# Performance work log

Hardware: AMD Instinct MI355X
Metric: run time of the kernel (lower is better)

The kernel has to match this reference:

```python
import jax
import jax.numpy as jnp
import numpy as np
from jax import lax

# Model dims (see init_kwargs)
B, C, D, M, L = 16, 64, 128, 16, 3
PROJ, OUT = 64, 1  # projection_size defaults to channels; output_size=1


def _spectral_conv(v, w1, w2, bias):
    """FNO 2D spectral convolution. v: [B,C,D,D]; w1,w2: [C,C,M,M,2] (re/im); bias: [C]."""
    vft = jnp.fft.rfft2(v, norm="backward")            # [B,C,D,D//2+1] complex
    w1c = w1[..., 0] + 1j * w1[..., 1]                   # [C,C,M,M]
    w2c = w2[..., 0] + 1j * w2[..., 1]
    top = jnp.einsum("bixy,ioxy->boxy", vft[:, :, :M, :M], w1c)
    bot = jnp.einsum("bixy,ioxy->boxy", vft[:, :, -M:, :M], w2c)
    out_ft = jnp.zeros_like(vft)
    out_ft = out_ft.at[:, :, :M, :M].set(top).at[:, :, -M:, :M].set(bot)
    out = jnp.fft.irfft2(out_ft, s=(D, D), norm="backward")
    return out + bias[None, :, None, None]               # in_bias


def _rk4(f, z0, ts):
    """Fixed-grid RK4 (torchdiffeq method='rk4'): one step per interval; return final state."""
    def step(z, tp):
        h = tp[1] - tp[0]
        k1 = f(z)
        k2 = f(z + 0.5 * h * k1)
        k3 = f(z + 0.5 * h * k2)
        k4 = f(z + h * k3)
        return z + (h / 6.0) * (k1 + 2.0 * k2 + 2.0 * k3 + k4), None
    pairs = jnp.stack([ts[:-1], ts[1:]], axis=1)         # [T-1, 2]
    zf, _ = lax.scan(step, z0, pairs)
    return zf


def setup_inputs() -> dict:
    key = jax.random.key(0)
    ks = jax.random.split(key, 12)
    scale = 1.0 / C                                       # FNO-style spectral weight scale
    z = jax.random.normal(ks[0], (B, 1, D, D), jnp.float32)
    lift_w = jax.random.normal(ks[1], (C, 1), jnp.float32)
    lift_b = jax.random.normal(ks[2], (C,), jnp.float32) * 0.1
    spec_w1 = jax.random.normal(ks[3], (L, C, C, M, M, 2), jnp.float32) * scale
    spec_w2 = jax.random.normal(ks[4], (L, C, C, M, M, 2), jnp.float32) * scale
    fl_bias = jax.random.normal(ks[5], (L, C), jnp.float32) * 0.1
    p1_w = jax.random.normal(ks[6], (PROJ, C), jnp.float32) / np.sqrt(C)
    p1_b = jax.random.normal(ks[7], (PROJ,), jnp.float32) * 0.1
    p2_w = jax.random.normal(ks[8], (OUT, PROJ), jnp.float32) / np.sqrt(PROJ)
    p2_b = jax.random.normal(ks[9], (OUT,), jnp.float32) * 0.1
    samp_ts = jnp.linspace(0.0, 1.0, 5, dtype=jnp.float32)
    return dict(z=z, lift_w=lift_w, lift_b=lift_b, spec_w1=spec_w1, spec_w2=spec_w2,
                fl_bias=fl_bias, p1_w=p1_w, p1_b=p1_b, p2_w=p2_w, p2_b=p2_b,
                samp_ts=samp_ts)


def reference(z, lift_w, lift_b, spec_w1, spec_w2, fl_bias, p1_w, p1_b, p2_w, p2_b, samp_ts):
    # Lifting: pointwise channel lift 1 -> C
    v = jnp.einsum("bixy,oi->boxy", z, lift_w) + lift_b[None, :, None, None]
    out = v
    # n_layers Fourier layers, each integrated with RK4 over samp_ts; take final time
    for l in range(L):
        f = lambda u, l=l: _spectral_conv(u, spec_w1[l], spec_w2[l], fl_bias[l])
        out = _rk4(f, out, samp_ts)
    # Projection: pointwise C -> PROJ -> OUT
    h = jnp.einsum("bcxy,pc->bpxy", out, p1_w) + p1_b[None, :, None, None]
    out = jnp.einsum("bpxy,op->boxy", h, p2_w) + p2_b[None, :, None, None]
    return out
```

## Files before the change

kernel.cpp:

```cpp
#include <hip/hip_runtime.h>

namespace {

constexpr int kNXI = 33;
constexpr int kNY = 16;
constexpr int kNMODE = kNY * kNXI;
constexpr int kModeBlocks = 265;
constexpr int kFwd1Blocks = 2048;

constexpr int WS_ALPHA = 0;
constexpr int WS_GAMMA = 1;
constexpr int WS_S = 4;
constexpr int WS_ZY = WS_S + kNMODE * 2;
constexpr int WS_T = WS_ZY;

constexpr float kTheta = 0.04908738521234052f;

__device__ __forceinline__ float rl(float v, int i) {
  return __uint_as_float(__builtin_amdgcn_readlane(__float_as_uint(v), i));
}

__device__ __forceinline__ float wave_sum(float v) {
  v += __shfl_xor(v, 1);  v += __shfl_xor(v, 2);  v += __shfl_xor(v, 4);
  v += __shfl_xor(v, 8);  v += __shfl_xor(v, 16); v += __shfl_xor(v, 32);
  return v;
}

__global__ __launch_bounds__(128) void fnde_phase1(
    const float* __restrict__ w1, const float* __restrict__ w2,
    const float* __restrict__ flb, const float* __restrict__ lw,
    const float* __restrict__ lb, const float* __restrict__ ts,
    const float* __restrict__ p1w, const float* __restrict__ p1b,
    const float* __restrict__ p2w, const float* __restrict__ p2b,
    const float* __restrict__ z, float* __restrict__ ws) {
  const int b = blockIdx.x;

  if (b >= kModeBlocks) {
    const int bid = b - kModeBlocks;
    const int bb = bid >> 7, xs = bid & 127;
    const int t = threadIdx.x;
    __shared__ float zrow[128], tc[128], tsn[128], rre[128], rim[128];
    sincosf((float)t * kTheta, &tsn[t], &tc[t]);
    zrow[t] = z[bb * 16384 + xs * 128 + t];
    __syncthreads();
    int y = t & 15, part = t >> 4;
    float sre = 0.f, sim = 0.f;
    for (int j = 0; j < 16; ++j) {
      int ys = (part << 4) + j;
      int k = (y * ys) & 127;
      float zv = zrow[ys];
      sre += zv * tc[k];
      sim -= zv * tsn[k];
    }
    rre[t] = sre; rim[t] = sim;
    __syncthreads();
    if (t < 16) {
      float ar = 0.f, ai = 0.f;
      for (int pp = 0; pp < 8; ++pp) { ar += rre[(pp << 4) + t]; ai += rim[(pp << 4) + t]; }
      int idx = ((bb * 128 + xs) * 16 + t) * 2;
      ws[WS_ZY + idx] = ar; ws[WS_ZY + idx + 1] = ai;
    }
    return;
  }

  const int t = threadIdx.x;
  const int o = t & 63, w = t >> 6;

  const float t0 = ts[0], t1 = ts[1], t2 = ts[2], t3 = ts[3], t4 = ts[4];
  const float h0 = t1 - t0, h1 = t2 - t1, h2 = t3 - t2, h3 = t4 - t3;

  if (b == kModeBlocks - 1) {
    if (w == 1) return;
    float q = 0.f;
    for (int p = 0; p < 64; ++p) q = fmaf(p2w[p], p1w[p * 64 + o], q);
    float e = lb[o];
    const float* lanep = w1 + o * 512;
    for (int l = 0; l < 3; ++l) {
      float Wc[64];
#pragma unroll
      for (int i = 0; i < 64; ++i) Wc[i] = lanep[(size_t)(l * 64 + i) * 32768];
      const float bia = flb[l * 64 + o];
      for (int step = 0; step < 4; ++step) {
        const float h = (step == 0) ? h0 : (step == 1) ? h1 : (step == 2) ? h2 : h3;
        float acc = 0.f, u = e;
        for (int st = 0; st < 4; ++st) {
          float k0 = 0.f, k1 = 0.f;
#pragma unroll
          for (int i = 0; i < 64; i += 2) {
            k0 = fmaf(Wc[i],     rl(u, i),     k0);
            k1 = fmaf(Wc[i + 1], rl(u, i + 1), k1);
          }
          const float k = k0 + k1 + bia;
          const float wsm = (st == 1 || st == 2) ? 2.f : 1.f;
          acc = fmaf(wsm, k, acc);
          if (st < 3) {
            const float cm = (st < 2) ? 0.5f * h : h;
            u = fmaf(cm, k, e);
          } else {
            e = fmaf(h * (1.f / 6.f), acc, e);
          }
        }
      }
    }
    const float g = wave_sum(fmaf(p2w[o], p1b[o], q * e));
    if (o == 0) ws[WS_GAMMA] = g + p2b[0];
    return;
  }

  const int xcd = b & 7, kk0 = (b >> 3) * 2 + w;
  int xi, y;
  if (kk0 < 64) { xi = xcd * 4 + (kk0 >> 4); y = kk0 & 15; }
  else          { xi = 32;                   y = xcd * 2 + (kk0 - 64); }
  const int m = y * kNXI + xi;

  const bool inactive = (y == 0) ? (xi > 16) : (xi == 16);
  if (inactive) {
    if (o == 0) { ws[WS_S + 2 * m] = 0.f; ws[WS_S + 2 * m + 1] = 0.f; }
    return;
  }

  float q = 0.f;
  for (int p = 0; p < 64; ++p) q = fmaf(p2w[p], p1w[p * 64 + o], q);

  float zr = lw[o], zi = 0.f;
  float2 Wc[64];

  for (int l = 0; l < 3; ++l) {
    if (y >= 1) {
      const float* lanep = ((xi <= 15) ? (w1 + (xi * 16 + y) * 2)
                                       : (w2 + ((xi - 17) * 16 + y) * 2)) + o * 512;
#pragma unroll
      for (int i = 0; i < 64; ++i)
        Wc[i] = *reinterpret_cast<const float2*>(lanep + (size_t)(l * 64 + i) * 32768);
    } else {
      const bool hasA = (xi <= 15);
      const float* lanepA = w1 + xi * 32 + o * 512;
      const float* lanepB = (xi >= 1) ? (w2 + (16 - xi) * 32 + o * 512)
                                      : (w1 + o * 512);
#pragma unroll
      for (int i = 0; i < 64; ++i) {
        const float2 a = hasA ? *reinterpret_cast<const float2*>(lanepA + (size_t)(l * 64 + i) * 32768)
                              : make_float2(0.f, 0.f);
        const float2 bb = *reinterpret_cast<const float2*>(lanepB + (size_t)(l * 64 + i) * 32768);
        Wc[i] = make_float2(0.5f * (a.x + bb.x), 0.5f * (a.y - bb.y));
      }
    }

    for (int step = 0; step < 4; ++step) {
      const float h = (step == 0) ? h0 : (step == 1) ? h1 : (step == 2) ? h2 : h3;
      float accr = 0.f, acci = 0.f;
      float ur = zr, ui = zi;
      for (int st = 0; st < 4; ++st) {
        float ar0 = 0.f, ai0 = 0.f, ar1 = 0.f, ai1 = 0.f;
#pragma unroll
        for (int i = 0; i < 64; i += 2) {
          const float x0r = rl(ur, i),     x0i = rl(ui, i);
          const float x1r = rl(ur, i + 1), x1i = rl(ui, i + 1);
          ar0 = fmaf(Wc[i].x,     x0r, ar0);  ar0 = fmaf(-Wc[i].y,     x0i, ar0);
          ai0 = fmaf(Wc[i].x,     x0i, ai0);  ai0 = fmaf(Wc[i].y,     x0r, ai0);
          ar1 = fmaf(Wc[i + 1].x, x1r, ar1);  ar1 = fmaf(-Wc[i + 1].y, x1i, ar1);
          ai1 = fmaf(Wc[i + 1].x, x1i, ai1);  ai1 = fmaf(Wc[i + 1].y,  x1r, ai1);
        }
        const float kr = ar0 + ar1, ki = ai0 + ai1;
        const float wsm = (st == 1 || st == 2) ? 2.f : 1.f;
        accr = fmaf(wsm, kr, accr); acci = fmaf(wsm, ki, acci);
        if (st < 3) {
          const float cm = (st < 2) ? 0.5f * h : h;
          ur = fmaf(cm, kr, zr); ui = fmaf(cm, ki, zi);
        } else {
          zr = fmaf(h * (1.f / 6.f), accr, zr);
          zi = fmaf(h * (1.f / 6.f), acci, zi);
        }
      }
    }
  }

  const float sr = wave_sum(q * (zr - lw[o]));
  const float si = wave_sum(q * zi);
  if (o == 0) { ws[WS_S + 2 * m] = sr; ws[WS_S + 2 * m + 1] = si; }
  if (y == 0 && xi == 0) {
    const float a = wave_sum(q * lw[o]);
    if (o == 0) ws[WS_ALPHA] = a;
  }
}

__global__ void fnde_mid(float* __restrict__ ws) {
  const int b = blockIdx.x >> 4, y = blockIdx.x & 15;
  const int t = threadIdx.x;
  __shared__ float cr[128], ci[128], tc[128], tsn[128], Sre[kNXI], Sim[kNXI];
  sincosf((float)t * kTheta, &tsn[t], &tc[t]);
  int idx = ((b * 128 + t) * 16 + y) * 2;
  cr[t] = ws[WS_ZY + idx]; ci[t] = ws[WS_ZY + idx + 1];
  __syncthreads();
  if (t < kNXI) {
    int x = (t <= 16) ? t : t + 95;
    float ar = 0.f, ai = 0.f;
    for (int xs = 0; xs < 128; ++xs) {
      int k = (x * xs) & 127;
      float c = tc[k], s = tsn[k];
      ar += cr[xs] * c + ci[xs] * s;
      ai += ci[xs] * c - cr[xs] * s;
    }
    int mm = y * kNXI + t;
    float sr = ws[WS_S + 2 * mm], si = ws[WS_S + 2 * mm + 1];
    Sre[t] = sr * ar - si * ai;
    Sim[t] = sr * ai + si * ar;
  }
  __syncthreads();
  const int xs = t;
  float ar, ai;
  if (y > 0) {
    ar = 0.f; ai = 0.f;
    for (int xj = 0; xj < kNXI; ++xj) {
      int x = (xj <= 16) ? xj : xj + 95;
      int k = (x * xs) & 127;
      float c = tc[k], s = tsn[k];
      ar += Sre[xj] * c - Sim[xj] * s;
      ai += Sre[xj] * s + Sim[xj] * c;
    }
  } else {
    ar = Sre[0]; ai = 0.f;
    for (int xj = 1; xj <= 16; ++xj) {
      int k = (xj * xs) & 127;
      ar += 2.f * (Sre[xj] * tc[k] - Sim[xj] * tsn[k]);
    }
  }
  ws[WS_T + idx] = ar; ws[WS_T + idx + 1] = ai;
}

__global__ void fnde_final(const float* __restrict__ z, const float* __restrict__ ws,
                           float* __restrict__ out) {
  const int bid = blockIdx.x;
  const int b = bid >> 7, xs = bid & 127;
  const int t = threadIdx.x;
  __shared__ float Tre[16], Tim[16], tc[128], tsn[128];
  sincosf((float)t * kTheta, &tsn[t], &tc[t]);
  if (t < 16) {
    int idx = ((b * 128 + xs) * 16 + t) * 2;
    Tre[t] = ws[WS_T + idx]; Tim[t] = ws[WS_T + idx + 1];
  }
  __syncthreads();
  float acc = Tre[0];
  for (int y = 1; y < 16; ++y) {
    int k = (y * t) & 127;
    acc += 2.f * (Tre[y] * tc[k] - Tim[y] * tsn[k]);
  }
  float val = ws[WS_ALPHA] * z[b * 16384 + xs * 128 + t] + ws[WS_GAMMA]
            + acc * (1.f / 16384.f);
  out[b * 16384 + xs * 128 + t] = val;
}

}

extern "C" void kernel_launch(void* const* d_in, const int* in_sizes, int n_in,
                              void* d_out, int out_size, void* d_ws, size_t ws_size,
                              hipStream_t stream) {
  (void)in_sizes; (void)n_in; (void)out_size; (void)ws_size;
  const float* z   = (const float*)d_in[0];
  const float* lw  = (const float*)d_in[1];
  const float* lb  = (const float*)d_in[2];
  const float* w1  = (const float*)d_in[3];
  const float* w2  = (const float*)d_in[4];
  const float* flb = (const float*)d_in[5];
  const float* p1w = (const float*)d_in[6];
  const float* p1b = (const float*)d_in[7];
  const float* p2w = (const float*)d_in[8];
  const float* p2b = (const float*)d_in[9];
  const float* ts  = (const float*)d_in[10];
  float* ws = (float*)d_ws;
  float* out = (float*)d_out;

  fnde_phase1<<<dim3(kModeBlocks + kFwd1Blocks), dim3(128), 0, stream>>>(
      w1, w2, flb, lw, lb, ts, p1w, p1b, p2w, p2b, z, ws);
  fnde_mid<<<dim3(256), dim3(128), 0, stream>>>(ws);
  fnde_final<<<dim3(2048), dim3(128), 0, stream>>>(z, ws, out);
}
```

Measured before the change: 94.57 us.

## Split per-mode channel matvec across four waves with LDS reduction

Each mode block now uses four waves, each holding 16 of the 64 input-channel weights instead of one wave holding all 64. Partial complex dot products are exchanged through shared memory with a barrier every RK4 stage, replacing readlane broadcasts. This cuts per-thread register use and serial FMA chain length so more waves can run in parallel. The forward-row blocks are also doubled up to two rows per block. The cost is a __syncthreads per stage (48 per block) and twice as many mode blocks.

```diff
diff --git a/kernel.cpp b/kernel.cpp
--- a/kernel.cpp
+++ b/kernel.cpp
@@ -5,8 +5,8 @@
 constexpr int kNXI = 33;
 constexpr int kNY = 16;
 constexpr int kNMODE = kNY * kNXI;
-constexpr int kModeBlocks = 265;
-constexpr int kFwd1Blocks = 2048;
+constexpr int kModeBlocks = 529;
+constexpr int kFwd1Blocks = 1024;
 
 constexpr int WS_ALPHA = 0;
 constexpr int WS_GAMMA = 1;
@@ -16,17 +16,13 @@
 
 constexpr float kTheta = 0.04908738521234052f;
 
-__device__ __forceinline__ float rl(float v, int i) {
-  return __uint_as_float(__builtin_amdgcn_readlane(__float_as_uint(v), i));
-}
-
 __device__ __forceinline__ float wave_sum(float v) {
   v += __shfl_xor(v, 1);  v += __shfl_xor(v, 2);  v += __shfl_xor(v, 4);
   v += __shfl_xor(v, 8);  v += __shfl_xor(v, 16); v += __shfl_xor(v, 32);
   return v;
 }
 
-__global__ __launch_bounds__(128) void fnde_phase1(
+__global__ __launch_bounds__(256) void fnde_phase1(
     const float* __restrict__ w1, const float* __restrict__ w2,
     const float* __restrict__ flb, const float* __restrict__ lw,
     const float* __restrict__ lb, const float* __restrict__ ts,
@@ -34,153 +30,151 @@
     const float* __restrict__ p2w, const float* __restrict__ p2b,
     const float* __restrict__ z, float* __restrict__ ws) {
   const int b = blockIdx.x;
+  const int t = threadIdx.x;
 
   if (b >= kModeBlocks) {
+    __shared__ float zrow2[2][128], tcf[128], tsnf[128], rre2[2][128], rim2[2][128];
     const int bid = b - kModeBlocks;
-    const int bb = bid >> 7, xs = bid & 127;
-    const int t = threadIdx.x;
-    __shared__ float zrow[128], tc[128], tsn[128], rre[128], rim[128];
-    sincosf((float)t * kTheta, &tsn[t], &tc[t]);
-    zrow[t] = z[bb * 16384 + xs * 128 + t];
+    const int r = t >> 7, tt = t & 127;
+    const int row = bid * 2 + r;
+    const int bb = row >> 7, xs = row & 127;
+    if (r == 0) sincosf((float)tt * kTheta, &tsnf[tt], &tcf[tt]);
+    zrow2[r][tt] = z[bb * 16384 + xs * 128 + tt];
     __syncthreads();
-    int y = t & 15, part = t >> 4;
+    int y = tt & 15, part = tt >> 4;
     float sre = 0.f, sim = 0.f;
     for (int j = 0; j < 16; ++j) {
       int ys = (part << 4) + j;
       int k = (y * ys) & 127;
-      float zv = zrow[ys];
-      sre += zv * tc[k];
-      sim -= zv * tsn[k];
-    }
-    rre[t] = sre; rim[t] = sim;
+      float zv = zrow2[r][ys];
+      sre += zv * tcf[k];
+      sim -= zv * tsnf[k];
+    }
+    rre2[r][tt] = sre; rim2[r][tt] = sim;
     __syncthreads();
-    if (t < 16) {
+    if (tt < 16) {
       float ar = 0.f, ai = 0.f;
-      for (int pp = 0; pp < 8; ++pp) { ar += rre[(pp << 4) + t]; ai += rim[(pp << 4) + t]; }
-      int idx = ((bb * 128 + xs) * 16 + t) * 2;
+      for (int pp = 0; pp < 8; ++pp) { ar += rre2[r][(pp << 4) + tt]; ai += rim2[r][(pp << 4) + tt]; }
+      int idx = (row * 16 + tt) * 2;
       ws[WS_ZY + idx] = ar; ws[WS_ZY + idx + 1] = ai;
     }
     return;
   }
 
-  const int t = threadIdx.x;
-  const int o = t & 63, w = t >> 6;
+  const int w = t >> 6, o = t & 63;
+  const bool isBias = (b == kModeBlocks - 1);
+
+  int xi = 0, y = 0, m = 0;
+  if (!isBias) {
+    const int xcd = b & 7, k = b >> 3;
+    if (k < 64) { xi = xcd * 4 + (k >> 4); y = k & 15; }
+    else        { xi = 32;                 y = xcd * 2 + (k - 64); }
+    m = y * kNXI + xi;
+    const bool inactive = (y == 0) ? (xi > 16) : (xi == 16);
+    if (inactive) {
+      if (t == 0) { ws[WS_S + 2 * m] = 0.f; ws[WS_S + 2 * m + 1] = 0.f; }
+      return;
+    }
+  }
+
+  __shared__ float2 ubuf[4][64];
+  __shared__ float2 pbuf[2][4][64];
 
   const float t0 = ts[0], t1 = ts[1], t2 = ts[2], t3 = ts[3], t4 = ts[4];
   const float h0 = t1 - t0, h1 = t2 - t1, h2 = t3 - t2, h3 = t4 - t3;
 
-  if (b == kModeBlocks - 1) {
-    if (w == 1) return;
-    float q = 0.f;
+  float q = 0.f;
+  if (w == 0) {
     for (int p = 0; p < 64; ++p) q = fmaf(p2w[p], p1w[p * 64 + o], q);
-    float e = lb[o];
-    const float* lanep = w1 + o * 512;
-    for (int l = 0; l < 3; ++l) {
-      float Wc[64];
-#pragma unroll
-      for (int i = 0; i < 64; ++i) Wc[i] = lanep[(size_t)(l * 64 + i) * 32768];
-      const float bia = flb[l * 64 + o];
-      for (int step = 0; step < 4; ++step) {
-        const float h = (step == 0) ? h0 : (step == 1) ? h1 : (step == 2) ? h2 : h3;
-        float acc = 0.f, u = e;
-        for (int st = 0; st < 4; ++st) {
-          float k0 = 0.f, k1 = 0.f;
-#pragma unroll
-          for (int i = 0; i < 64; i += 2) {
-            k0 = fmaf(Wc[i],     rl(u, i),     k0);
-            k1 = fmaf(Wc[i + 1], rl(u, i + 1), k1);
-          }
-          const float k = k0 + k1 + bia;
-          const float wsm = (st == 1 || st == 2) ? 2.f : 1.f;
-          acc = fmaf(wsm, k, acc);
-          if (st < 3) {
-            const float cm = (st < 2) ? 0.5f * h : h;
-            u = fmaf(cm, k, e);
-          } else {
-            e = fmaf(h * (1.f / 6.f), acc, e);
-          }
-        }
-      }
-    }
-    const float g = wave_sum(fmaf(p2w[o], p1b[o], q * e));
-    if (o == 0) ws[WS_GAMMA] = g + p2b[0];
-    return;
-  }
-
-  const int xcd = b & 7, kk0 = (b >> 3) * 2 + w;
-  int xi, y;
-  if (kk0 < 64) { xi = xcd * 4 + (kk0 >> 4); y = kk0 & 15; }
-  else          { xi = 32;                   y = xcd * 2 + (kk0 - 64); }
-  const int m = y * kNXI + xi;
-
-  const bool inactive = (y == 0) ? (xi > 16) : (xi == 16);
-  if (inactive) {
-    if (o == 0) { ws[WS_S + 2 * m] = 0.f; ws[WS_S + 2 * m + 1] = 0.f; }
-    return;
-  }
-
-  float q = 0.f;
-  for (int p = 0; p < 64; ++p) q = fmaf(p2w[p], p1w[p * 64 + o], q);
-
-  float zr = lw[o], zi = 0.f;
-  float2 Wc[64];
+  }
+
+  float zr = isBias ? lb[o] : lw[o], zi = 0.f;
+  ubuf[w][o] = make_float2(zr, zi);
+
+  int pb = 0;
+  float2 Wc[16];
 
   for (int l = 0; l < 3; ++l) {
-    if (y >= 1) {
+    if (isBias) {
+      const float* lanep = w1 + o * 512;
+#pragma unroll
+      for (int j = 0; j < 16; ++j)
+        Wc[j] = make_float2(lanep[(size_t)(l * 64 + 16 * w + j) * 32768], 0.f);
+    } else if (y >= 1) {
       const float* lanep = ((xi <= 15) ? (w1 + (xi * 16 + y) * 2)
                                        : (w2 + ((xi - 17) * 16 + y) * 2)) + o * 512;
 #pragma unroll
-      for (int i = 0; i < 64; ++i)
-        Wc[i] = *reinterpret_cast<const float2*>(lanep + (size_t)(l * 64 + i) * 32768);
+      for (int j = 0; j < 16; ++j)
+        Wc[j] = *reinterpret_cast<const float2*>(lanep + (size_t)(l * 64 + 16 * w + j) * 32768);
     } else {
       const bool hasA = (xi <= 15);
       const float* lanepA = w1 + xi * 32 + o * 512;
       const float* lanepB = (xi >= 1) ? (w2 + (16 - xi) * 32 + o * 512)
                                       : (w1 + o * 512);
 #pragma unroll
-      for (int i = 0; i < 64; ++i) {
-        const float2 a = hasA ? *reinterpret_cast<const float2*>(lanepA + (size_t)(l * 64 + i) * 32768)
+      for (int j = 0; j < 16; ++j) {
+        const size_t ioff = (size_t)(l * 64 + 16 * w + j) * 32768;
+        const float2 a = hasA ? *reinterpret_cast<const float2*>(lanepA + ioff)
                               : make_float2(0.f, 0.f);
-        const float2 bb = *reinterpret_cast<const float2*>(lanepB + (size_t)(l * 64 + i) * 32768);
-        Wc[i] = make_float2(0.5f * (a.x + bb.x), 0.5f * (a.y - bb.y));
+        const float2 bb2 = *reinterpret_cast<const float2*>(lanepB + ioff);
+        Wc[j] = make_float2(0.5f * (a.x + bb2.x), 0.5f * (a.y - bb2.y));
       }
     }
+    const float bia = isBias ? flb[l * 64 + o] : 0.f;
 
     for (int step = 0; step < 4; ++step) {
       const float h = (step == 0) ? h0 : (step == 1) ? h1 : (step == 2) ? h2 : h3;
       float accr = 0.f, acci = 0.f;
-      float ur = zr, ui = zi;
       for (int st = 0; st < 4; ++st) {
-        float ar0 = 0.f, ai0 = 0.f, ar1 = 0.f, ai1 = 0.f;
-#pragma unroll
-        for (int i = 0; i < 64; i += 2) {
-          const float x0r = rl(ur, i),     x0i = rl(ui, i);
-          const float x1r = rl(ur, i + 1), x1i = rl(ui, i + 1);
-          ar0 = fmaf(Wc[i].x,     x0r, ar0);  ar0 = fmaf(-Wc[i].y,     x0i, ar0);
-          ai0 = fmaf(Wc[i].x,     x0i, ai0);  ai0 = fmaf(Wc[i].y,     x0r, ai0);
-          ar1 = fmaf(Wc[i + 1].x, x1r, ar1);  ar1 = fmaf(-Wc[i + 1].y, x1i, ar1);
-          ai1 = fmaf(Wc[i + 1].x, x1i, ai1);  ai1 = fmaf(Wc[i + 1].y,  x1r, ai1);
+        float2 x[16];
+#pragma unroll
+        for (int jj = 0; jj < 8; ++jj)
+          *reinterpret_cast<float4*>(&x[2 * jj]) =
+              *reinterpret_cast<const float4*>(&ubuf[w][16 * w + 2 * jj]);
+        float pr0 = 0.f, pi0 = 0.f, pr1 = 0.f, pi1 = 0.f;
+#pragma unroll
+        for (int j = 0; j < 16; j += 2) {
+          pr0 = fmaf(Wc[j].x,     x[j].x,     pr0);  pr0 = fmaf(-Wc[j].y,     x[j].y,     pr0);
+          pi0 = fmaf(Wc[j].x,     x[j].y,     pi0);  pi0 = fmaf(Wc[j].y,      x[j].x,     pi0);
+          pr1 = fmaf(Wc[j + 1].x, x[j + 1].x, pr1);  pr1 = fmaf(-Wc[j + 1].y, x[j + 1].y, pr1);
+          pi1 = fmaf(Wc[j + 1].x, x[j + 1].y, pi1);  pi1 = fmaf(Wc[j + 1].y,  x[j + 1].x, pi1);
         }
-        const float kr = ar0 + ar1, ki = ai0 + ai1;
+        pbuf[pb][w][o] = make_float2(pr0 + pr1, pi0 + pi1);
+        __syncthreads();
+        const float2 q0 = pbuf[pb][0][o], q1 = pbuf[pb][1][o];
+        const float2 q2 = pbuf[pb][2][o], q3 = pbuf[pb][3][o];
+        const float kr = q0.x + q1.x + q2.x + q3.x + bia;
+        const float ki = q0.y + q1.y + q2.y + q3.y;
         const float wsm = (st == 1 || st == 2) ? 2.f : 1.f;
         accr = fmaf(wsm, kr, accr); acci = fmaf(wsm, ki, acci);
+        float ur, ui;
         if (st < 3) {
           const float cm = (st < 2) ? 0.5f * h : h;
           ur = fmaf(cm, kr, zr); ui = fmaf(cm, ki, zi);
         } else {
           zr = fmaf(h * (1.f / 6.f), accr, zr);
           zi = fmaf(h * (1.f / 6.f), acci, zi);
+          ur = zr; ui = zi;
         }
+        ubuf[w][o] = make_float2(ur, ui);
+        pb ^= 1;
       }
     }
   }
 
-  const float sr = wave_sum(q * (zr - lw[o]));
-  const float si = wave_sum(q * zi);
-  if (o == 0) { ws[WS_S + 2 * m] = sr; ws[WS_S + 2 * m + 1] = si; }
-  if (y == 0 && xi == 0) {
-    const float a = wave_sum(q * lw[o]);
-    if (o == 0) ws[WS_ALPHA] = a;
+  if (w == 0) {
+    if (isBias) {
+      const float g = wave_sum(fmaf(p2w[o], p1b[o], q * zr));
+      if (o == 0) ws[WS_GAMMA] = g + p2b[0];
+    } else {
+      const float sr = wave_sum(q * (zr - lw[o]));
+      const float si = wave_sum(q * zi);
+      if (o == 0) { ws[WS_S + 2 * m] = sr; ws[WS_S + 2 * m + 1] = si; }
+      if (m == 0) {
+        const float a = wave_sum(q * lw[o]);
+        if (o == 0) ws[WS_ALPHA] = a;
+      }
+    }
   }
 }
 
@@ -270,7 +264,7 @@
   float* ws = (float*)d_ws;
   float* out = (float*)d_out;
 
-  fnde_phase1<<<dim3(kModeBlocks + kFwd1Blocks), dim3(128), 0, stream>>>(
+  fnde_phase1<<<dim3(kModeBlocks + kFwd1Blocks), dim3(256), 0, stream>>>(
       w1, w2, flb, lw, lb, ts, p1w, p1b, p2w, p2b, z, ws);
   fnde_mid<<<dim3(256), dim3(128), 0, stream>>>(ws);
   fnde_final<<<dim3(2048), dim3(128), 0, stream>>>(z, ws, out);
```

Result: no change. 94.48 us (-0.1%).

## Use one-wave blocks and LDS broadcast instead of readlane in mode RK4

Applied to the files above, without the earlier changes.

Each phase-1 block is now a single 64-lane wave, and the number of mode blocks is doubled so each block handles one Fourier mode. Inside the per-mode RK4 matvec, the per-lane readlane broadcasts are replaced by each lane writing its state into shared memory and all lanes reading it back as float4 vectors. The forward row-DFT blocks also shrink to 64 threads, with the partial-sum reduction done by cross-lane shuffles instead of a shared-memory pass. The aim is to avoid the serialized scalar readlane path and to spread work over more blocks. The cost is more LDS traffic, and correctness relies on in-wave ordering of LDS accesses because there is no barrier.

```diff
diff --git a/kernel.cpp b/kernel.cpp
--- a/kernel.cpp
+++ b/kernel.cpp
@@ -5,7 +5,7 @@
 constexpr int kNXI = 33;
 constexpr int kNY = 16;
 constexpr int kNMODE = kNY * kNXI;
-constexpr int kModeBlocks = 265;
+constexpr int kModeBlocks = 529;
 constexpr int kFwd1Blocks = 2048;
 
 constexpr int WS_ALPHA = 0;
@@ -16,17 +16,13 @@
 
 constexpr float kTheta = 0.04908738521234052f;
 
-__device__ __forceinline__ float rl(float v, int i) {
-  return __uint_as_float(__builtin_amdgcn_readlane(__float_as_uint(v), i));
-}
-
 __device__ __forceinline__ float wave_sum(float v) {
   v += __shfl_xor(v, 1);  v += __shfl_xor(v, 2);  v += __shfl_xor(v, 4);
   v += __shfl_xor(v, 8);  v += __shfl_xor(v, 16); v += __shfl_xor(v, 32);
   return v;
 }
 
-__global__ __launch_bounds__(128) void fnde_phase1(
+__global__ __launch_bounds__(64, 1) void fnde_phase1(
     const float* __restrict__ w1, const float* __restrict__ w2,
     const float* __restrict__ flb, const float* __restrict__ lw,
     const float* __restrict__ lb, const float* __restrict__ ts,
@@ -34,71 +30,84 @@
     const float* __restrict__ p2w, const float* __restrict__ p2b,
     const float* __restrict__ z, float* __restrict__ ws) {
   const int b = blockIdx.x;
+  const int o = threadIdx.x;
 
   if (b >= kModeBlocks) {
-    const int bid = b - kModeBlocks;
-    const int bb = bid >> 7, xs = bid & 127;
-    const int t = threadIdx.x;
-    __shared__ float zrow[128], tc[128], tsn[128], rre[128], rim[128];
-    sincosf((float)t * kTheta, &tsn[t], &tc[t]);
-    zrow[t] = z[bb * 16384 + xs * 128 + t];
-    __syncthreads();
-    int y = t & 15, part = t >> 4;
+    __shared__ float zrow[128], tcf[128], tsnf[128];
+    const int row = b - kModeBlocks;
+    const int bb = row >> 7, xs = row & 127;
+    sincosf((float)o * kTheta, &tsnf[o], &tcf[o]);
+    sincosf((float)(o + 64) * kTheta, &tsnf[o + 64], &tcf[o + 64]);
+    const float* zp = z + bb * 16384 + xs * 128;
+    zrow[o] = zp[o]; zrow[o + 64] = zp[o + 64];
+    const int y = o & 15, part = o >> 4;
     float sre = 0.f, sim = 0.f;
-    for (int j = 0; j < 16; ++j) {
-      int ys = (part << 4) + j;
-      int k = (y * ys) & 127;
-      float zv = zrow[ys];
-      sre += zv * tc[k];
-      sim -= zv * tsn[k];
-    }
-    rre[t] = sre; rim[t] = sim;
-    __syncthreads();
-    if (t < 16) {
-      float ar = 0.f, ai = 0.f;
-      for (int pp = 0; pp < 8; ++pp) { ar += rre[(pp << 4) + t]; ai += rim[(pp << 4) + t]; }
-      int idx = ((bb * 128 + xs) * 16 + t) * 2;
-      ws[WS_ZY + idx] = ar; ws[WS_ZY + idx + 1] = ai;
+    for (int j = 0; j < 32; ++j) {
+      const int ys = (part << 5) + j;
+      const int k = (y * ys) & 127;
+      const float zv = zrow[ys];
+      sre = fmaf(zv, tcf[k], sre);
+      sim = fmaf(-zv, tsnf[k], sim);
+    }
+    sre += __shfl_xor(sre, 16); sre += __shfl_xor(sre, 32);
+    sim += __shfl_xor(sim, 16); sim += __shfl_xor(sim, 32);
+    if (o < 16) {
+      const int idx = (row * 16 + o) * 2;
+      ws[WS_ZY + idx] = sre; ws[WS_ZY + idx + 1] = sim;
     }
     return;
   }
 
-  const int t = threadIdx.x;
-  const int o = t & 63, w = t >> 6;
+  const bool isBias = (b == kModeBlocks - 1);
+
+  int xi = 0, y = 0, m = 0;
+  if (!isBias) {
+    const int xcd = b & 7, k = b >> 3;
+    if (k < 64) { xi = xcd * 4 + (k >> 4); y = k & 15; }
+    else        { xi = 32;                 y = xcd * 2 + (k - 64); }
+    m = y * kNXI + xi;
+    const bool inactive = (y == 0) ? (xi > 16) : (xi == 16);
+    if (inactive) {
+      if (o == 0) { ws[WS_S + 2 * m] = 0.f; ws[WS_S + 2 * m + 1] = 0.f; }
+      return;
+    }
+  }
+
+  __shared__ __align__(16) float2 xb[64];
 
   const float t0 = ts[0], t1 = ts[1], t2 = ts[2], t3 = ts[3], t4 = ts[4];
   const float h0 = t1 - t0, h1 = t2 - t1, h2 = t3 - t2, h3 = t4 - t3;
 
-  if (b == kModeBlocks - 1) {
-    if (w == 1) return;
-    float q = 0.f;
-    for (int p = 0; p < 64; ++p) q = fmaf(p2w[p], p1w[p * 64 + o], q);
+  float q = 0.f;
+  for (int p = 0; p < 64; ++p) q = fmaf(p2w[p], p1w[p * 64 + o], q);
+
+  if (isBias) {
     float e = lb[o];
+    xb[o] = make_float2(e, 0.f);
     const float* lanep = w1 + o * 512;
     for (int l = 0; l < 3; ++l) {
-      float Wc[64];
-#pragma unroll
-      for (int i = 0; i < 64; ++i) Wc[i] = lanep[(size_t)(l * 64 + i) * 32768];
+      float Wr[64];
+#pragma unroll
+      for (int i = 0; i < 64; ++i) Wr[i] = lanep[(size_t)(l * 64 + i) * 32768];
       const float bia = flb[l * 64 + o];
       for (int step = 0; step < 4; ++step) {
         const float h = (step == 0) ? h0 : (step == 1) ? h1 : (step == 2) ? h2 : h3;
-        float acc = 0.f, u = e;
+        float acc = 0.f;
         for (int st = 0; st < 4; ++st) {
           float k0 = 0.f, k1 = 0.f;
 #pragma unroll
-          for (int i = 0; i < 64; i += 2) {
-            k0 = fmaf(Wc[i],     rl(u, i),     k0);
-            k1 = fmaf(Wc[i + 1], rl(u, i + 1), k1);
+          for (int ii = 0; ii < 64; ii += 2) {
+            const float4 xx = *reinterpret_cast<const float4*>(&xb[ii]);
+            k0 = fmaf(Wr[ii],     xx.x, k0);
+            k1 = fmaf(Wr[ii + 1], xx.z, k1);
           }
-          const float k = k0 + k1 + bia;
+          const float kk = k0 + k1 + bia;
           const float wsm = (st == 1 || st == 2) ? 2.f : 1.f;
-          acc = fmaf(wsm, k, acc);
-          if (st < 3) {
-            const float cm = (st < 2) ? 0.5f * h : h;
-            u = fmaf(cm, k, e);
-          } else {
-            e = fmaf(h * (1.f / 6.f), acc, e);
-          }
+          acc = fmaf(wsm, kk, acc);
+          float u;
+          if (st < 3) { const float cm = (st < 2) ? 0.5f * h : h; u = fmaf(cm, kk, e); }
+          else        { e = fmaf(h * (1.f / 6.f), acc, e); u = e; }
+          xb[o] = make_float2(u, 0.f);
         }
       }
     }
@@ -107,22 +116,9 @@
     return;
   }
 
-  const int xcd = b & 7, kk0 = (b >> 3) * 2 + w;
-  int xi, y;
-  if (kk0 < 64) { xi = xcd * 4 + (kk0 >> 4); y = kk0 & 15; }
-  else          { xi = 32;                   y = xcd * 2 + (kk0 - 64); }
-  const int m = y * kNXI + xi;
-
-  const bool inactive = (y == 0) ? (xi > 16) : (xi == 16);
-  if (inactive) {
-    if (o == 0) { ws[WS_S + 2 * m] = 0.f; ws[WS_S + 2 * m + 1] = 0.f; }
-    return;
-  }
-
-  float q = 0.f;
-  for (int p = 0; p < 64; ++p) q = fmaf(p2w[p], p1w[p * 64 + o], q);
-
   float zr = lw[o], zi = 0.f;
+  xb[o] = make_float2(zr, zi);
+
   float2 Wc[64];
 
   for (int l = 0; l < 3; ++l) {
@@ -139,38 +135,40 @@
                                       : (w1 + o * 512);
 #pragma unroll
       for (int i = 0; i < 64; ++i) {
-        const float2 a = hasA ? *reinterpret_cast<const float2*>(lanepA + (size_t)(l * 64 + i) * 32768)
+        const size_t ioff = (size_t)(l * 64 + i) * 32768;
+        const float2 a = hasA ? *reinterpret_cast<const float2*>(lanepA + ioff)
                               : make_float2(0.f, 0.f);
-        const float2 bb = *reinterpret_cast<const float2*>(lanepB + (size_t)(l * 64 + i) * 32768);
-        Wc[i] = make_float2(0.5f * (a.x + bb.x), 0.5f * (a.y - bb.y));
+        const float2 bb2 = *reinterpret_cast<const float2*>(lanepB + ioff);
+        Wc[i] = make_float2(0.5f * (a.x + bb2.x), 0.5f * (a.y - bb2.y));
       }
     }
 
     for (int step = 0; step < 4; ++step) {
       const float h = (step == 0) ? h0 : (step == 1) ? h1 : (step == 2) ? h2 : h3;
       float accr = 0.f, acci = 0.f;
-      float ur = zr, ui = zi;
       for (int st = 0; st < 4; ++st) {
         float ar0 = 0.f, ai0 = 0.f, ar1 = 0.f, ai1 = 0.f;
 #pragma unroll
-        for (int i = 0; i < 64; i += 2) {
-          const float x0r = rl(ur, i),     x0i = rl(ui, i);
-          const float x1r = rl(ur, i + 1), x1i = rl(ui, i + 1);
-          ar0 = fmaf(Wc[i].x,     x0r, ar0);  ar0 = fmaf(-Wc[i].y,     x0i, ar0);
-          ai0 = fmaf(Wc[i].x,     x0i, ai0);  ai0 = fmaf(Wc[i].y,     x0r, ai0);
-          ar1 = fmaf(Wc[i + 1].x, x1r, ar1);  ar1 = fmaf(-Wc[i + 1].y, x1i, ar1);
-          ai1 = fmaf(Wc[i + 1].x, x1i, ai1);  ai1 = fmaf(Wc[i + 1].y,  x1r, ai1);
+        for (int ii = 0; ii < 64; ii += 2) {
+          const float4 xx = *reinterpret_cast<const float4*>(&xb[ii]);
+          ar0 = fmaf(Wc[ii].x,     xx.x, ar0);  ar0 = fmaf(-Wc[ii].y,     xx.y, ar0);
+          ai0 = fmaf(Wc[ii].x,     xx.y, ai0);  ai0 = fmaf(Wc[ii].y,      xx.x, ai0);
+          ar1 = fmaf(Wc[ii + 1].x, xx.z, ar1);  ar1 = fmaf(-Wc[ii + 1].y, xx.w, ar1);
+          ai1 = fmaf(Wc[ii + 1].x, xx.w, ai1);  ai1 = fmaf(Wc[ii + 1].y,  xx.z, ai1);
         }
         const float kr = ar0 + ar1, ki = ai0 + ai1;
         const float wsm = (st == 1 || st == 2) ? 2.f : 1.f;
         accr = fmaf(wsm, kr, accr); acci = fmaf(wsm, ki, acci);
+        float ur, ui;
         if (st < 3) {
           const float cm = (st < 2) ? 0.5f * h : h;
           ur = fmaf(cm, kr, zr); ui = fmaf(cm, ki, zi);
         } else {
           zr = fmaf(h * (1.f / 6.f), accr, zr);
           zi = fmaf(h * (1.f / 6.f), acci, zi);
+          ur = zr; ui = zi;
         }
+        xb[o] = make_float2(ur, ui);
       }
     }
   }
@@ -178,7 +176,7 @@
   const float sr = wave_sum(q * (zr - lw[o]));
   const float si = wave_sum(q * zi);
   if (o == 0) { ws[WS_S + 2 * m] = sr; ws[WS_S + 2 * m + 1] = si; }
-  if (y == 0 && xi == 0) {
+  if (m == 0) {
     const float a = wave_sum(q * lw[o]);
     if (o == 0) ws[WS_ALPHA] = a;
   }
@@ -270,7 +268,7 @@
   float* ws = (float*)d_ws;
   float* out = (float*)d_out;
 
-  fnde_phase1<<<dim3(kModeBlocks + kFwd1Blocks), dim3(128), 0, stream>>>(
+  fnde_phase1<<<dim3(kModeBlocks + kFwd1Blocks), dim3(64), 0, stream>>>(
       w1, w2, flb, lw, lb, ts, p1w, p1b, p2w, p2b, z, ws);
   fnde_mid<<<dim3(256), dim3(128), 0, stream>>>(ws);
   fnde_final<<<dim3(2048), dim3(128), 0, stream>>>(z, ws, out);
```

New measurement: 227.6 us. 141% more time.
